# Kernel optimization log

Measured on AMD Instinct MI355X. Metric: run time of the kernel, lower is better.

Reference implementation:

```python
import jax, jax.numpy as jnp
import numpy as np

N = 50000   # n_nodes
E = 800000  # n_edges (directed)
D = 64      # feature dim (in = hidden = out = 64 per source)


def setup_inputs() -> dict:
    key = jax.random.key(0)
    ks = jax.random.split(key, 16)
    s = 0.1  # init scale
    inp = {
        "x": jax.random.normal(ks[0], (N, D), jnp.float32),
        "edge_index": jax.random.randint(ks[1], (2, E), 0, N),
        # GCNConv 1
        "W1": jax.random.normal(ks[2], (D, 64), jnp.float32) * s,
        "b1": jnp.zeros((64,), jnp.float32),
        # TransformerConv (heads=1): query/key/value + root (skip) linear
        "Wq": jax.random.normal(ks[3], (64, 64), jnp.float32) * s,
        "bq": jnp.zeros((64,), jnp.float32),
        "Wk": jax.random.normal(ks[4], (64, 64), jnp.float32) * s,
        "bk": jnp.zeros((64,), jnp.float32),
        "Wv": jax.random.normal(ks[5], (64, 64), jnp.float32) * s,
        "bv": jnp.zeros((64,), jnp.float32),
        "Ws": jax.random.normal(ks[6], (64, 64), jnp.float32) * s,
        "bs": jnp.zeros((64,), jnp.float32),
        # GCNConv 2
        "W2": jax.random.normal(ks[7], (64, D), jnp.float32) * s,
        "b2": jnp.zeros((D,), jnp.float32),
    }
    return inp


def gcn_conv(x, W, b, src, dst, n):
    """PyG GCNConv: symmetric normalization with self-loops, then scatter-add."""
    xw = x @ W  # [N, F]
    loop = jnp.arange(n)
    src2 = jnp.concatenate([src, loop])
    dst2 = jnp.concatenate([dst, loop])
    deg = jax.ops.segment_sum(jnp.ones(src2.shape[0], xw.dtype), dst2, num_segments=n)
    dinv = jnp.where(deg > 0, jax.lax.rsqrt(deg), 0.0)
    norm = dinv[src2] * dinv[dst2]  # [E+N]
    out = jax.ops.segment_sum(xw[src2] * norm[:, None], dst2, num_segments=n)
    return out + b


def segment_softmax(logits, seg, n):
    m = jax.ops.segment_max(logits, seg, num_segments=n)
    e = jnp.exp(logits - m[seg])
    z = jax.ops.segment_sum(e, seg, num_segments=n)
    return e / z[seg]


def transformer_conv(x, Wq, bq, Wk, bk, Wv, bv, Ws, bs, src, dst, n):
    """PyG TransformerConv (heads=1, concat=True, root_weight=True)."""
    q = x @ Wq + bq  # [N, 64]
    k = x @ Wk + bk
    v = x @ Wv + bv
    scale = jax.lax.rsqrt(jnp.asarray(q.shape[-1], q.dtype))
    logits = jnp.sum(q[dst] * k[src], axis=-1) * scale  # [E]
    alpha = segment_softmax(logits, dst, n)
    aggr = jax.ops.segment_sum(v[src] * alpha[:, None], dst, num_segments=n)
    return aggr + x @ Ws + bs  # root/skip connection


def reference(x, edge_index, W1, b1, Wq, bq, Wk, bk, Wv, bv, Ws, bs, W2, b2):
    src, dst = edge_index[0], edge_index[1]
    n = x.shape[0]
    x1 = jax.nn.relu(gcn_conv(x, W1, b1, src, dst, n))
    x2 = transformer_conv(x1, Wq, bq, Wk, bk, Wv, bv, Ws, bs, src, dst, n)
    x3 = gcn_conv(x2, W2, b2, src, dst, n)
    return x3
```

## Files before the change

kernel.cpp:

```cpp
#include <hip/hip_runtime.h>
#include <math.h>


#define D 64
#define BKT_SHIFT 9
#define CAP 12288
#define CHUNK 4096

__device__ __forceinline__ unsigned short f2bf(float f) {
    unsigned int u = __float_as_uint(f);
    u += 0x7FFFu + ((u >> 16) & 1u);
    return (unsigned short)(u >> 16);
}
#define BF_LO(u) __uint_as_float((u) << 16)
#define BF_HI(u) __uint_as_float((u) & 0xFFFF0000u)


__global__ void init_gcursor(int* __restrict__ gcursor) {
    if (threadIdx.x < 128) gcursor[threadIdx.x] = 0;
}

__global__ __launch_bounds__(256) void binA_kernel(const int* __restrict__ src,
                                                   const int* __restrict__ dst,
                                                   int* __restrict__ gcursor,
                                                   unsigned int* __restrict__ staging,
                                                   int e, int nbkt) {
    __shared__ int cntB[128];
    __shared__ int offB[128];
    __shared__ int curB[128];
    __shared__ int gbase[128];
    __shared__ unsigned int pairs[CHUNK];
    __shared__ unsigned char bkt[CHUNK];

    int t = threadIdx.x;
    int e0 = blockIdx.x * CHUNK;
    int ecnt = min(CHUNK, e - e0);

    if (t < 128) cntB[t] = 0;
    __syncthreads();

    int myS[CHUNK / 256], myD[CHUNK / 256];
    #pragma unroll
    for (int i = 0; i < CHUNK / 256; ++i) {
        int idx = t + 256 * i;
        if (idx < ecnt) {
            myS[i] = src[e0 + idx];
            myD[i] = dst[e0 + idx];
            atomicAdd(&cntB[myD[i] >> BKT_SHIFT], 1);
        }
    }
    __syncthreads();
    if (t < 128) offB[t] = cntB[t];
    __syncthreads();
    for (int off = 1; off < 128; off <<= 1) {
        int add = (t < 128 && t >= off) ? offB[t - off] : 0;
        __syncthreads();
        if (t < 128) offB[t] += add;
        __syncthreads();
    }
    if (t < 128) {
        int excl = offB[t] - cntB[t];
        offB[t] = excl;
        curB[t] = excl;
        if (t < nbkt && cntB[t] > 0) gbase[t] = atomicAdd(&gcursor[t], cntB[t]);
    }
    __syncthreads();
    #pragma unroll
    for (int i = 0; i < CHUNK / 256; ++i) {
        int idx = t + 256 * i;
        if (idx < ecnt) {
            int b = myD[i] >> BKT_SHIFT;
            int p = atomicAdd(&curB[b], 1);
            pairs[p] = ((unsigned int)myD[i] << 16) | (unsigned int)myS[i];
            bkt[p] = (unsigned char)b;
        }
    }
    __syncthreads();
    for (int p = t; p < ecnt; p += 256) {
        int b = bkt[p];
        staging[(size_t)b * CAP + gbase[b] + (p - offB[b])] = pairs[p];
    }
}

__global__ __launch_bounds__(256) void binB_kernel(const int* __restrict__ gcursor,
                                                   const unsigned int* __restrict__ staging,
                                                   unsigned short* __restrict__ esrc,
                                                   int* __restrict__ cnt,
                                                   int* __restrict__ rowptr,
                                                   float* __restrict__ dinv,
                                                   int n, int nbkt) {
    __shared__ int bpre[128];
    __shared__ int c512[512];
    __shared__ int o512[512];
    int t = threadIdx.x;
    int b = blockIdx.x;

    if (t < 128) bpre[t] = (t < nbkt) ? gcursor[t] : 0;
    __syncthreads();
    for (int off = 1; off < 128; off <<= 1) {
        int add = (t < 128 && t >= off) ? bpre[t - off] : 0;
        __syncthreads();
        if (t < 128) bpre[t] += add;
        __syncthreads();
    }
    int base_b = (b == 0) ? 0 : bpre[b - 1];
    int cnt_b = gcursor[b];
    int lo = b << BKT_SHIFT;

    c512[t] = 0; c512[t + 256] = 0;
    __syncthreads();
    const unsigned int* st = staging + (size_t)b * CAP;
    for (int i = t; i < cnt_b; i += 256)
        atomicAdd(&c512[(int)(st[i] >> 16) - lo], 1);
    __syncthreads();
    o512[t] = c512[t]; o512[t + 256] = c512[t + 256];
    __syncthreads();
    for (int off = 1; off < 512; off <<= 1) {
        int a1 = (t >= off) ? o512[t - off] : 0;
        int a2 = o512[t + 256 - off];
        __syncthreads();
        o512[t] += a1; o512[t + 256] += a2;
        __syncthreads();
    }
    int e1 = o512[t] - c512[t];
    int e2 = o512[t + 256] - c512[t + 256];
    __syncthreads();
    o512[t] = e1; o512[t + 256] = e2;
    __syncthreads();
    for (int i = t; i < 512; i += 256) {
        int g = lo + i;
        if (g < n) {
            int c = c512[i];
            cnt[g] = c;
            rowptr[g] = base_b + o512[i];
            dinv[g] = rsqrtf((float)c + 1.0f);
        }
    }
    __syncthreads();
    for (int i = t; i < cnt_b; i += 256) {
        unsigned int pk = st[i];
        int local = (int)(pk >> 16) - lo;
        int p = atomicAdd(&o512[local], 1);
        esrc[base_b + p] = (unsigned short)(pk & 0xFFFFu);
    }
}

__global__ __launch_bounds__(256) void gemm64_bf16s(const float* __restrict__ X,
                                                    const float* __restrict__ W,
                                                    const float* __restrict__ dinv,
                                                    unsigned short* __restrict__ xs, int n) {
    __shared__ float sX[64][68];
    __shared__ float sW[64 * 64];
    int t = threadIdx.x;
    int base = blockIdx.x * 64;
    #pragma unroll
    for (int i = 0; i < 4; ++i) {
        int f = t * 4 + i * 1024;
        *(float4*)&sW[f] = *(const float4*)&W[f];
        int r = f >> 6, c = f & 63;
        int row = base + r;
        float4 xv = (row < n) ? *(const float4*)&X[(size_t)row * D + c]
                              : make_float4(0.f, 0.f, 0.f, 0.f);
        *(float4*)&sX[r][c] = xv;
    }
    __syncthreads();

    int cg = t & 15, rg = t >> 4;
    int j0 = cg * 4, r0 = rg * 4;
    float acc[4][4];
    #pragma unroll
    for (int a = 0; a < 4; ++a)
        #pragma unroll
        for (int c = 0; c < 4; ++c) acc[a][c] = 0.0f;

    #pragma unroll 4
    for (int kk = 0; kk < 64; kk += 4) {
        float4 w0 = *(const float4*)&sW[(kk + 0) * 64 + j0];
        float4 w1 = *(const float4*)&sW[(kk + 1) * 64 + j0];
        float4 w2 = *(const float4*)&sW[(kk + 2) * 64 + j0];
        float4 w3 = *(const float4*)&sW[(kk + 3) * 64 + j0];
        #pragma unroll
        for (int a = 0; a < 4; ++a) {
            float4 xv = *(const float4*)&sX[r0 + a][kk];
            acc[a][0] = fmaf(xv.x, w0.x, acc[a][0]); acc[a][1] = fmaf(xv.x, w0.y, acc[a][1]);
            acc[a][2] = fmaf(xv.x, w0.z, acc[a][2]); acc[a][3] = fmaf(xv.x, w0.w, acc[a][3]);
            acc[a][0] = fmaf(xv.y, w1.x, acc[a][0]); acc[a][1] = fmaf(xv.y, w1.y, acc[a][1]);
            acc[a][2] = fmaf(xv.y, w1.z, acc[a][2]); acc[a][3] = fmaf(xv.y, w1.w, acc[a][3]);
            acc[a][0] = fmaf(xv.z, w2.x, acc[a][0]); acc[a][1] = fmaf(xv.z, w2.y, acc[a][1]);
            acc[a][2] = fmaf(xv.z, w2.z, acc[a][2]); acc[a][3] = fmaf(xv.z, w2.w, acc[a][3]);
            acc[a][0] = fmaf(xv.w, w3.x, acc[a][0]); acc[a][1] = fmaf(xv.w, w3.y, acc[a][1]);
            acc[a][2] = fmaf(xv.w, w3.z, acc[a][2]); acc[a][3] = fmaf(xv.w, w3.w, acc[a][3]);
        }
    }

    #pragma unroll
    for (int a = 0; a < 4; ++a) {
        int row = base + r0 + a;
        if (row < n) {
            float dv = dinv[row];
            ushort4 h;
            h.x = f2bf(acc[a][0] * dv);
            h.y = f2bf(acc[a][1] * dv);
            h.z = f2bf(acc[a][2] * dv);
            h.w = f2bf(acc[a][3] * dv);
            *(ushort4*)&xs[(size_t)row * D + j0] = h;
        }
    }
}

__global__ __launch_bounds__(256) void gemm_qkvs(const float* __restrict__ X,
                                                 const float* __restrict__ Wq,
                                                 const float* __restrict__ bq,
                                                 const float* __restrict__ Wk,
                                                 const float* __restrict__ bk,
                                                 const float* __restrict__ Wv,
                                                 const float* __restrict__ bv,
                                                 const float* __restrict__ Ws,
                                                 const float* __restrict__ bs,
                                                 float* __restrict__ Yq,
                                                 unsigned short* __restrict__ kv,
                                                 float* __restrict__ Ysk, int n) {
    __shared__ float sX[64][68];
    __shared__ float sW[64 * 64];
    int t = threadIdx.x;
    int base = blockIdx.x * 64;
    #pragma unroll
    for (int i = 0; i < 4; ++i) {
        int f = t * 4 + i * 1024;
        int r = f >> 6, c = f & 63;
        int row = base + r;
        float4 xv = (row < n) ? *(const float4*)&X[(size_t)row * D + c]
                              : make_float4(0.f, 0.f, 0.f, 0.f);
        *(float4*)&sX[r][c] = xv;
    }

    int cg = t & 15, rg = t >> 4;
    int j0 = cg * 4, r0 = rg * 4;

    #pragma unroll 1
    for (int w4 = 0; w4 < 4; ++w4) {
        const float* W = (w4 == 0) ? Wq : (w4 == 1) ? Wk : (w4 == 2) ? Wv : Ws;
        const float* B = (w4 == 0) ? bq : (w4 == 1) ? bk : (w4 == 2) ? bv : bs;
        __syncthreads();
        #pragma unroll
        for (int i = 0; i < 4; ++i) {
            int f = t * 4 + i * 1024;
            *(float4*)&sW[f] = *(const float4*)&W[f];
        }
        __syncthreads();

        float acc[4][4];
        #pragma unroll
        for (int a = 0; a < 4; ++a)
            #pragma unroll
            for (int c = 0; c < 4; ++c) acc[a][c] = 0.0f;

        #pragma unroll 4
        for (int kk = 0; kk < 64; kk += 4) {
            float4 w0 = *(const float4*)&sW[(kk + 0) * 64 + j0];
            float4 w1 = *(const float4*)&sW[(kk + 1) * 64 + j0];
            float4 w2 = *(const float4*)&sW[(kk + 2) * 64 + j0];
            float4 w3 = *(const float4*)&sW[(kk + 3) * 64 + j0];
            #pragma unroll
            for (int a = 0; a < 4; ++a) {
                float4 xv = *(const float4*)&sX[r0 + a][kk];
                acc[a][0] = fmaf(xv.x, w0.x, acc[a][0]); acc[a][1] = fmaf(xv.x, w0.y, acc[a][1]);
                acc[a][2] = fmaf(xv.x, w0.z, acc[a][2]); acc[a][3] = fmaf(xv.x, w0.w, acc[a][3]);
                acc[a][0] = fmaf(xv.y, w1.x, acc[a][0]); acc[a][1] = fmaf(xv.y, w1.y, acc[a][1]);
                acc[a][2] = fmaf(xv.y, w1.z, acc[a][2]); acc[a][3] = fmaf(xv.y, w1.w, acc[a][3]);
                acc[a][0] = fmaf(xv.z, w2.x, acc[a][0]); acc[a][1] = fmaf(xv.z, w2.y, acc[a][1]);
                acc[a][2] = fmaf(xv.z, w2.z, acc[a][2]); acc[a][3] = fmaf(xv.z, w2.w, acc[a][3]);
                acc[a][0] = fmaf(xv.w, w3.x, acc[a][0]); acc[a][1] = fmaf(xv.w, w3.y, acc[a][1]);
                acc[a][2] = fmaf(xv.w, w3.z, acc[a][2]); acc[a][3] = fmaf(xv.w, w3.w, acc[a][3]);
            }
        }

        float4 bb = *(const float4*)&B[j0];
        if (w4 == 0) {
            #pragma unroll
            for (int a = 0; a < 4; ++a) {
                int row = base + r0 + a;
                if (row < n) {
                    float4 o = make_float4((acc[a][0] + bb.x) * 0.125f,
                                           (acc[a][1] + bb.y) * 0.125f,
                                           (acc[a][2] + bb.z) * 0.125f,
                                           (acc[a][3] + bb.w) * 0.125f);
                    *(float4*)&Yq[(size_t)row * D + j0] = o;
                }
            }
        } else if (w4 == 3) {
            #pragma unroll
            for (int a = 0; a < 4; ++a) {
                int row = base + r0 + a;
                if (row < n) {
                    float4 o = make_float4(acc[a][0] + bb.x, acc[a][1] + bb.y,
                                           acc[a][2] + bb.z, acc[a][3] + bb.w);
                    *(float4*)&Ysk[(size_t)row * D + j0] = o;
                }
            }
        } else {
            int off = (w4 == 1) ? 0 : 64;
            #pragma unroll
            for (int a = 0; a < 4; ++a) {
                int row = base + r0 + a;
                if (row < n) {
                    ushort4 h;
                    h.x = f2bf(acc[a][0] + bb.x);
                    h.y = f2bf(acc[a][1] + bb.y);
                    h.z = f2bf(acc[a][2] + bb.z);
                    h.w = f2bf(acc[a][3] + bb.w);
                    *(ushort4*)&kv[(size_t)row * 128 + off + j0] = h;
                }
            }
        }
    }
}

__global__ __launch_bounds__(256) void gcn_gather_kernel(const unsigned short* __restrict__ xs,
                                                         const float* __restrict__ dinv,
                                                         const int* __restrict__ rowptr,
                                                         const int* __restrict__ cnt,
                                                         const unsigned short* __restrict__ esrc,
                                                         const float* __restrict__ bias,
                                                         float* __restrict__ out,
                                                         int n, int relu) {
    int node = (blockIdx.x * blockDim.x + threadIdx.x) >> 6;
    if (node >= n) return;
    int lane = threadIdx.x & 63;
    int grp = lane >> 3;
    int sub = lane & 7;
    int j0 = sub * 8;

    int start = rowptr[node], deg = cnt[node];

    float a[8] = {0.f, 0.f, 0.f, 0.f, 0.f, 0.f, 0.f, 0.f};
    int i = grp;
    int sNext = (i < deg) ? esrc[start + i] : 0;
    for (; i < deg; i += 8) {
        int s = sNext;
        int in = i + 8;
        if (in < deg) sNext = esrc[start + in];
        uint4 r = *(const uint4*)&xs[(size_t)s * D + j0];
        a[0] += BF_LO(r.x); a[1] += BF_HI(r.x);
        a[2] += BF_LO(r.y); a[3] += BF_HI(r.y);
        a[4] += BF_LO(r.z); a[5] += BF_HI(r.z);
        a[6] += BF_LO(r.w); a[7] += BF_HI(r.w);
    }
    #pragma unroll
    for (int off = 8; off < 64; off <<= 1) {
        #pragma unroll
        for (int c = 0; c < 8; ++c) a[c] += __shfl_xor(a[c], off, 64);
    }

    if (grp == 0) {
        float dd = dinv[node];
        uint4 sr = *(const uint4*)&xs[(size_t)node * D + j0];
        a[0] += BF_LO(sr.x); a[1] += BF_HI(sr.x);
        a[2] += BF_LO(sr.y); a[3] += BF_HI(sr.y);
        a[4] += BF_LO(sr.z); a[5] += BF_HI(sr.z);
        a[6] += BF_LO(sr.w); a[7] += BF_HI(sr.w);
        float4 b0 = *(const float4*)&bias[j0];
        float4 b1 = *(const float4*)&bias[j0 + 4];
        float o[8];
        o[0] = fmaf(dd, a[0], b0.x); o[1] = fmaf(dd, a[1], b0.y);
        o[2] = fmaf(dd, a[2], b0.z); o[3] = fmaf(dd, a[3], b0.w);
        o[4] = fmaf(dd, a[4], b1.x); o[5] = fmaf(dd, a[5], b1.y);
        o[6] = fmaf(dd, a[6], b1.z); o[7] = fmaf(dd, a[7], b1.w);
        if (relu) {
            #pragma unroll
            for (int c = 0; c < 8; ++c) o[c] = fmaxf(o[c], 0.f);
        }
        *(float4*)&out[(size_t)node * D + j0] = make_float4(o[0], o[1], o[2], o[3]);
        *(float4*)&out[(size_t)node * D + j0 + 4] = make_float4(o[4], o[5], o[6], o[7]);
    }
}

__global__ __launch_bounds__(256) void attn_gather_kernel(const float* __restrict__ q,
                                                          const unsigned short* __restrict__ kv,
                                                          const float* __restrict__ skip,
                                                          const int* __restrict__ rowptr,
                                                          const int* __restrict__ cnt,
                                                          const unsigned short* __restrict__ esrc,
                                                          float* __restrict__ out, int n) {
    int node = (blockIdx.x * blockDim.x + threadIdx.x) >> 6;
    if (node >= n) return;
    int lane = threadIdx.x & 63;
    int grp = lane >> 3;
    int sub = lane & 7;
    int j0 = sub * 8;

    int start = rowptr[node], deg = cnt[node];
    float4 q0 = *(const float4*)&q[(size_t)node * D + j0];
    float4 q1 = *(const float4*)&q[(size_t)node * D + j0 + 4];

    float m = -INFINITY, z = 0.0f;
    float a[8] = {0.f, 0.f, 0.f, 0.f, 0.f, 0.f, 0.f, 0.f};

    int i = grp;
    int sNext = (i < deg) ? esrc[start + i] : 0;
    for (; i < deg; i += 8) {
        int s = sNext;
        int in = i + 8;
        if (in < deg) sNext = esrc[start + in];
        const unsigned short* row = kv + (size_t)s * 128;
        uint4 kr = *(const uint4*)&row[j0];
        uint4 vr = *(const uint4*)&row[64 + j0];
        float p = q0.x * BF_LO(kr.x) + q0.y * BF_HI(kr.x)
                + q0.z * BF_LO(kr.y) + q0.w * BF_HI(kr.y)
                + q1.x * BF_LO(kr.z) + q1.y * BF_HI(kr.z)
                + q1.z * BF_LO(kr.w) + q1.w * BF_HI(kr.w);
        p += __shfl_xor(p, 1, 64);
        p += __shfl_xor(p, 2, 64);
        p += __shfl_xor(p, 4, 64);
        float l = p;
        float mn = fmaxf(m, l);
        float corr = __expf(m - mn);
        float w = __expf(l - mn);
        z = z * corr + w;
        a[0] = fmaf(w, BF_LO(vr.x), a[0] * corr);
        a[1] = fmaf(w, BF_HI(vr.x), a[1] * corr);
        a[2] = fmaf(w, BF_LO(vr.y), a[2] * corr);
        a[3] = fmaf(w, BF_HI(vr.y), a[3] * corr);
        a[4] = fmaf(w, BF_LO(vr.z), a[4] * corr);
        a[5] = fmaf(w, BF_HI(vr.z), a[5] * corr);
        a[6] = fmaf(w, BF_LO(vr.w), a[6] * corr);
        a[7] = fmaf(w, BF_HI(vr.w), a[7] * corr);
        m = mn;
    }

    float4 s0 = (grp == 0) ? *(const float4*)&skip[(size_t)node * D + j0]
                           : make_float4(0.f, 0.f, 0.f, 0.f);
    float4 s1 = (grp == 0) ? *(const float4*)&skip[(size_t)node * D + j0 + 4]
                           : make_float4(0.f, 0.f, 0.f, 0.f);

    if (deg > 0) {
        float M = m;
        M = fmaxf(M, __shfl_xor(M, 8, 64));
        M = fmaxf(M, __shfl_xor(M, 16, 64));
        M = fmaxf(M, __shfl_xor(M, 32, 64));
        float sc = __expf(m - M);
        float zs = z * sc;
        #pragma unroll
        for (int c = 0; c < 8; ++c) a[c] *= sc;
        #pragma unroll
        for (int off = 8; off < 64; off <<= 1) {
            zs += __shfl_xor(zs, off, 64);
            #pragma unroll
            for (int c = 0; c < 8; ++c) a[c] += __shfl_xor(a[c], off, 64);
        }
        if (grp == 0) {
            float inv = 1.0f / zs;
            float4 o0, o1;
            o0.x = fmaf(a[0], inv, s0.x); o0.y = fmaf(a[1], inv, s0.y);
            o0.z = fmaf(a[2], inv, s0.z); o0.w = fmaf(a[3], inv, s0.w);
            o1.x = fmaf(a[4], inv, s1.x); o1.y = fmaf(a[5], inv, s1.y);
            o1.z = fmaf(a[6], inv, s1.z); o1.w = fmaf(a[7], inv, s1.w);
            *(float4*)&out[(size_t)node * D + j0] = o0;
            *(float4*)&out[(size_t)node * D + j0 + 4] = o1;
        }
    } else if (grp == 0) {
        *(float4*)&out[(size_t)node * D + j0] = s0;
        *(float4*)&out[(size_t)node * D + j0 + 4] = s1;
    }
}


extern "C" void kernel_launch(void* const* d_in, const int* in_sizes, int n_in,
                              void* d_out, int out_size, void* d_ws, size_t ws_size,
                              hipStream_t stream) {
    const float* x  = (const float*)d_in[0];
    const int*   ei = (const int*)d_in[1];
    const float* W1 = (const float*)d_in[2];
    const float* b1 = (const float*)d_in[3];
    const float* Wq = (const float*)d_in[4];
    const float* bq = (const float*)d_in[5];
    const float* Wk = (const float*)d_in[6];
    const float* bk = (const float*)d_in[7];
    const float* Wv = (const float*)d_in[8];
    const float* bv = (const float*)d_in[9];
    const float* Ws = (const float*)d_in[10];
    const float* bs = (const float*)d_in[11];
    const float* W2 = (const float*)d_in[12];
    const float* b2 = (const float*)d_in[13];
    float* out = (float*)d_out;

    const int n = in_sizes[0] / D;
    const int e = in_sizes[1] / 2;
    const int* src = ei;
    const int* dst = ei + e;
    const int n64 = n * D;
    const int nbkt = (n + (1 << BKT_SHIFT) - 1) >> BKT_SHIFT;

    char* w = (char*)d_ws;
    auto carve = [&](size_t bytes) {
        char* p = w;
        w += (bytes + 255) & ~(size_t)255;
        return p;
    };
    int* gcursor            = (int*)carve(128 * 4);
    unsigned int* staging   = (unsigned int*)carve((size_t)nbkt * CAP * 4);
    unsigned short* esrc    = (unsigned short*)carve((size_t)e * 2);
    int* cnt                = (int*)carve((size_t)n * 4);
    int* rowptr             = (int*)carve((size_t)n * 4);
    float* dinv             = (float*)carve((size_t)n * 4);
    float* bufA             = (float*)carve((size_t)n64 * 4);
    float* bufB             = (float*)carve((size_t)n64 * 4);
    unsigned short* xs      = (unsigned short*)carve((size_t)n64 * 2);
    unsigned short* kv      = (unsigned short*)carve((size_t)n64 * 4);

    const int nb_binA = (e + CHUNK - 1) / CHUNK;
    const int nb_nw   = (n + 3) / 4;
    const int nb_g    = (n + 63) / 64;

    init_gcursor<<<1, 128, 0, stream>>>(gcursor);
    binA_kernel<<<nb_binA, 256, 0, stream>>>(src, dst, gcursor, staging, e, nbkt);
    binB_kernel<<<nbkt, 256, 0, stream>>>(gcursor, staging, esrc, cnt, rowptr, dinv, n, nbkt);

    gemm64_bf16s<<<nb_g, 256, 0, stream>>>(x, W1, dinv, xs, n);
    gcn_gather_kernel<<<nb_nw, 256, 0, stream>>>(xs, dinv, rowptr, cnt, esrc,
                                                 b1, bufB, n, 1);

    gemm_qkvs<<<nb_g, 256, 0, stream>>>(bufB, Wq, bq, Wk, bk, Wv, bv, Ws, bs,
                                        bufA, kv, out, n);
    attn_gather_kernel<<<nb_nw, 256, 0, stream>>>(bufA, kv, out,
                                                  rowptr, cnt, esrc, bufB, n);

    gemm64_bf16s<<<nb_g, 256, 0, stream>>>(bufB, W2, dinv, xs, n);
    gcn_gather_kernel<<<nb_nw, 256, 0, stream>>>(xs, dinv, rowptr, cnt, esrc,
                                                 b2, out, n, 0);
}
```

Before: 254.9 us.

## Fuse GCN/attention gathers into the following GEMM kernels per 64-node tile

The first GCN aggregation (with bias and ReLU) is fused into the Q/K/V/skip GEMM, and the attention aggregation is fused into the W2 GEMM. Each gathered 64-node tile goes straight into shared memory instead of round-tripping full fp32 node-feature buffers through global memory, and two launches are removed. Each node is now handled by 8 lanes that walk all of its edges serially, where before 64 lanes split a node's edges across 8 groups. That gives longer dependent gather loops and fewer waves to hide memory latency.

```diff
diff --git a/kernel.cpp b/kernel.cpp
--- a/kernel.cpp
+++ b/kernel.cpp
@@ -208,34 +208,74 @@
     }
 }
 
-__global__ __launch_bounds__(256) void gemm_qkvs(const float* __restrict__ X,
-                                                 const float* __restrict__ Wq,
-                                                 const float* __restrict__ bq,
-                                                 const float* __restrict__ Wk,
-                                                 const float* __restrict__ bk,
-                                                 const float* __restrict__ Wv,
-                                                 const float* __restrict__ bv,
-                                                 const float* __restrict__ Ws,
-                                                 const float* __restrict__ bs,
-                                                 float* __restrict__ Yq,
-                                                 unsigned short* __restrict__ kv,
-                                                 float* __restrict__ Ysk, int n) {
+__global__ __launch_bounds__(256) void fusedA_kernel(const unsigned short* __restrict__ xs,
+                                                     const float* __restrict__ dinv,
+                                                     const int* __restrict__ rowptr,
+                                                     const int* __restrict__ cnt,
+                                                     const unsigned short* __restrict__ esrc,
+                                                     const float* __restrict__ b1,
+                                                     const float* __restrict__ Wq,
+                                                     const float* __restrict__ bq,
+                                                     const float* __restrict__ Wk,
+                                                     const float* __restrict__ bk,
+                                                     const float* __restrict__ Wv,
+                                                     const float* __restrict__ bv,
+                                                     const float* __restrict__ Ws,
+                                                     const float* __restrict__ bs,
+                                                     float* __restrict__ Yq,
+                                                     unsigned short* __restrict__ kv,
+                                                     float* __restrict__ Ysk, int n) {
     __shared__ float sX[64][68];
     __shared__ float sW[64 * 64];
     int t = threadIdx.x;
     int base = blockIdx.x * 64;
-    #pragma unroll
-    for (int i = 0; i < 4; ++i) {
-        int f = t * 4 + i * 1024;
-        int r = f >> 6, c = f & 63;
-        int row = base + r;
-        float4 xv = (row < n) ? *(const float4*)&X[(size_t)row * D + c]
-                              : make_float4(0.f, 0.f, 0.f, 0.f);
-        *(float4*)&sX[r][c] = xv;
+    int wid = t >> 6, lane = t & 63;
+    int grp = lane >> 3, sub = lane & 7;
+    int j0 = sub * 8;
+
+    float4 bb0 = *(const float4*)&b1[j0];
+    float4 bb1 = *(const float4*)&b1[j0 + 4];
+
+    #pragma unroll
+    for (int slot = 0; slot < 2; ++slot) {
+        int local = wid * 16 + slot * 8 + grp;
+        int node = base + local;
+        float a[8] = {0.f, 0.f, 0.f, 0.f, 0.f, 0.f, 0.f, 0.f};
+        float4 o0 = make_float4(0.f, 0.f, 0.f, 0.f);
+        float4 o1 = make_float4(0.f, 0.f, 0.f, 0.f);
+        if (node < n) {
+            float dd = dinv[node];
+            int start = rowptr[node], deg = cnt[node];
+            uint4 sr = *(const uint4*)&xs[(size_t)node * D + j0];
+            a[0] += BF_LO(sr.x); a[1] += BF_HI(sr.x);
+            a[2] += BF_LO(sr.y); a[3] += BF_HI(sr.y);
+            a[4] += BF_LO(sr.z); a[5] += BF_HI(sr.z);
+            a[6] += BF_LO(sr.w); a[7] += BF_HI(sr.w);
+            int sNext = (deg > 0) ? esrc[start] : 0;
+            for (int i = 0; i < deg; ++i) {
+                int s = sNext;
+                if (i + 1 < deg) sNext = esrc[start + i + 1];
+                uint4 r = *(const uint4*)&xs[(size_t)s * D + j0];
+                a[0] += BF_LO(r.x); a[1] += BF_HI(r.x);
+                a[2] += BF_LO(r.y); a[3] += BF_HI(r.y);
+                a[4] += BF_LO(r.z); a[5] += BF_HI(r.z);
+                a[6] += BF_LO(r.w); a[7] += BF_HI(r.w);
+            }
+            o0.x = fmaxf(fmaf(dd, a[0], bb0.x), 0.f);
+            o0.y = fmaxf(fmaf(dd, a[1], bb0.y), 0.f);
+            o0.z = fmaxf(fmaf(dd, a[2], bb0.z), 0.f);
+            o0.w = fmaxf(fmaf(dd, a[3], bb0.w), 0.f);
+            o1.x = fmaxf(fmaf(dd, a[4], bb1.x), 0.f);
+            o1.y = fmaxf(fmaf(dd, a[5], bb1.y), 0.f);
+            o1.z = fmaxf(fmaf(dd, a[6], bb1.z), 0.f);
+            o1.w = fmaxf(fmaf(dd, a[7], bb1.w), 0.f);
+        }
+        *(float4*)&sX[local][j0] = o0;
+        *(float4*)&sX[local][j0 + 4] = o1;
     }
 
     int cg = t & 15, rg = t >> 4;
-    int j0 = cg * 4, r0 = rg * 4;
+    int gj0 = cg * 4, r0 = rg * 4;
 
     #pragma unroll 1
     for (int w4 = 0; w4 < 4; ++w4) {
@@ -257,10 +297,10 @@
 
         #pragma unroll 4
         for (int kk = 0; kk < 64; kk += 4) {
-            float4 w0 = *(const float4*)&sW[(kk + 0) * 64 + j0];
-            float4 w1 = *(const float4*)&sW[(kk + 1) * 64 + j0];
-            float4 w2 = *(const float4*)&sW[(kk + 2) * 64 + j0];
-            float4 w3 = *(const float4*)&sW[(kk + 3) * 64 + j0];
+            float4 w0 = *(const float4*)&sW[(kk + 0) * 64 + gj0];
+            float4 w1 = *(const float4*)&sW[(kk + 1) * 64 + gj0];
+            float4 w2 = *(const float4*)&sW[(kk + 2) * 64 + gj0];
+            float4 w3 = *(const float4*)&sW[(kk + 3) * 64 + gj0];
             #pragma unroll
             for (int a = 0; a < 4; ++a) {
                 float4 xv = *(const float4*)&sX[r0 + a][kk];
@@ -275,7 +315,7 @@
             }
         }
 
-        float4 bb = *(const float4*)&B[j0];
+        float4 bb = *(const float4*)&B[gj0];
         if (w4 == 0) {
             #pragma unroll
             for (int a = 0; a < 4; ++a) {
@@ -285,7 +325,7 @@
                                            (acc[a][1] + bb.y) * 0.125f,
                                            (acc[a][2] + bb.z) * 0.125f,
                                            (acc[a][3] + bb.w) * 0.125f);
-                    *(float4*)&Yq[(size_t)row * D + j0] = o;
+                    *(float4*)&Yq[(size_t)row * D + gj0] = o;
                 }
             }
         } else if (w4 == 3) {
@@ -295,7 +335,7 @@
                 if (row < n) {
                     float4 o = make_float4(acc[a][0] + bb.x, acc[a][1] + bb.y,
                                            acc[a][2] + bb.z, acc[a][3] + bb.w);
-                    *(float4*)&Ysk[(size_t)row * D + j0] = o;
+                    *(float4*)&Ysk[(size_t)row * D + gj0] = o;
                 }
             }
         } else {
@@ -309,9 +349,132 @@
                     h.y = f2bf(acc[a][1] + bb.y);
                     h.z = f2bf(acc[a][2] + bb.z);
                     h.w = f2bf(acc[a][3] + bb.w);
-                    *(ushort4*)&kv[(size_t)row * 128 + off + j0] = h;
+                    *(ushort4*)&kv[(size_t)row * 128 + off + gj0] = h;
                 }
             }
+        }
+    }
+}
+
+__global__ __launch_bounds__(256) void fusedB_kernel(const float* __restrict__ q,
+                                                     const unsigned short* __restrict__ kv,
+                                                     const float* __restrict__ skip,
+                                                     const float* __restrict__ dinv,
+                                                     const int* __restrict__ rowptr,
+                                                     const int* __restrict__ cnt,
+                                                     const unsigned short* __restrict__ esrc,
+                                                     const float* __restrict__ W2,
+                                                     unsigned short* __restrict__ xs2, int n) {
+    __shared__ float sX[64][68];
+    __shared__ float sW[64 * 64];
+    int t = threadIdx.x;
+    int base = blockIdx.x * 64;
+    int wid = t >> 6, lane = t & 63;
+    int grp = lane >> 3, sub = lane & 7;
+    int j0 = sub * 8;
+
+    #pragma unroll
+    for (int i = 0; i < 4; ++i) {
+        int f = t * 4 + i * 1024;
+        *(float4*)&sW[f] = *(const float4*)&W2[f];
+    }
+
+    #pragma unroll
+    for (int slot = 0; slot < 2; ++slot) {
+        int local = wid * 16 + slot * 8 + grp;
+        int node = base + local;
+        float4 o0 = make_float4(0.f, 0.f, 0.f, 0.f);
+        float4 o1 = make_float4(0.f, 0.f, 0.f, 0.f);
+        if (node < n) {
+            int start = rowptr[node], deg = cnt[node];
+            float4 q0 = *(const float4*)&q[(size_t)node * D + j0];
+            float4 q1 = *(const float4*)&q[(size_t)node * D + j0 + 4];
+            float4 s0 = *(const float4*)&skip[(size_t)node * D + j0];
+            float4 s1 = *(const float4*)&skip[(size_t)node * D + j0 + 4];
+            float m = -INFINITY, z = 0.0f;
+            float a[8] = {0.f, 0.f, 0.f, 0.f, 0.f, 0.f, 0.f, 0.f};
+            int sNext = (deg > 0) ? esrc[start] : 0;
+            for (int i = 0; i < deg; ++i) {
+                int s = sNext;
+                if (i + 1 < deg) sNext = esrc[start + i + 1];
+                const unsigned short* row = kv + (size_t)s * 128;
+                uint4 kr = *(const uint4*)&row[j0];
+                uint4 vr = *(const uint4*)&row[64 + j0];
+                float p = q0.x * BF_LO(kr.x) + q0.y * BF_HI(kr.x)
+                        + q0.z * BF_LO(kr.y) + q0.w * BF_HI(kr.y)
+                        + q1.x * BF_LO(kr.z) + q1.y * BF_HI(kr.z)
+                        + q1.z * BF_LO(kr.w) + q1.w * BF_HI(kr.w);
+                p += __shfl_xor(p, 1, 64);
+                p += __shfl_xor(p, 2, 64);
+                p += __shfl_xor(p, 4, 64);
+                float mn = fmaxf(m, p);
+                float corr = __expf(m - mn);
+                float w = __expf(p - mn);
+                z = z * corr + w;
+                a[0] = fmaf(w, BF_LO(vr.x), a[0] * corr);
+                a[1] = fmaf(w, BF_HI(vr.x), a[1] * corr);
+                a[2] = fmaf(w, BF_LO(vr.y), a[2] * corr);
+                a[3] = fmaf(w, BF_HI(vr.y), a[3] * corr);
+                a[4] = fmaf(w, BF_LO(vr.z), a[4] * corr);
+                a[5] = fmaf(w, BF_HI(vr.z), a[5] * corr);
+                a[6] = fmaf(w, BF_LO(vr.w), a[6] * corr);
+                a[7] = fmaf(w, BF_HI(vr.w), a[7] * corr);
+                m = mn;
+            }
+            if (deg > 0) {
+                float inv = 1.0f / z;
+                o0.x = fmaf(a[0], inv, s0.x); o0.y = fmaf(a[1], inv, s0.y);
+                o0.z = fmaf(a[2], inv, s0.z); o0.w = fmaf(a[3], inv, s0.w);
+                o1.x = fmaf(a[4], inv, s1.x); o1.y = fmaf(a[5], inv, s1.y);
+                o1.z = fmaf(a[6], inv, s1.z); o1.w = fmaf(a[7], inv, s1.w);
+            } else {
+                o0 = s0; o1 = s1;
+            }
+        }
+        *(float4*)&sX[local][j0] = o0;
+        *(float4*)&sX[local][j0 + 4] = o1;
+    }
+    __syncthreads();
+
+    int cg = t & 15, rg = t >> 4;
+    int gj0 = cg * 4, r0 = rg * 4;
+    float acc[4][4];
+    #pragma unroll
+    for (int a = 0; a < 4; ++a)
+        #pragma unroll
+        for (int c = 0; c < 4; ++c) acc[a][c] = 0.0f;
+
+    #pragma unroll 4
+    for (int kk = 0; kk < 64; kk += 4) {
+        float4 w0 = *(const float4*)&sW[(kk + 0) * 64 + gj0];
+        float4 w1 = *(const float4*)&sW[(kk + 1) * 64 + gj0];
+        float4 w2 = *(const float4*)&sW[(kk + 2) * 64 + gj0];
+        float4 w3 = *(const float4*)&sW[(kk + 3) * 64 + gj0];
+        #pragma unroll
+        for (int a = 0; a < 4; ++a) {
+            float4 xv = *(const float4*)&sX[r0 + a][kk];
+            acc[a][0] = fmaf(xv.x, w0.x, acc[a][0]); acc[a][1] = fmaf(xv.x, w0.y, acc[a][1]);
+            acc[a][2] = fmaf(xv.x, w0.z, acc[a][2]); acc[a][3] = fmaf(xv.x, w0.w, acc[a][3]);
+            acc[a][0] = fmaf(xv.y, w1.x, acc[a][0]); acc[a][1] = fmaf(xv.y, w1.y, acc[a][1]);
+            acc[a][2] = fmaf(xv.y, w1.z, acc[a][2]); acc[a][3] = fmaf(xv.y, w1.w, acc[a][3]);
+            acc[a][0] = fmaf(xv.z, w2.x, acc[a][0]); acc[a][1] = fmaf(xv.z, w2.y, acc[a][1]);
+            acc[a][2] = fmaf(xv.z, w2.z, acc[a][2]); acc[a][3] = fmaf(xv.z, w2.w, acc[a][3]);
+            acc[a][0] = fmaf(xv.w, w3.x, acc[a][0]); acc[a][1] = fmaf(xv.w, w3.y, acc[a][1]);
+            acc[a][2] = fmaf(xv.w, w3.z, acc[a][2]); acc[a][3] = fmaf(xv.w, w3.w, acc[a][3]);
+        }
+    }
+
+    #pragma unroll
+    for (int a = 0; a < 4; ++a) {
+        int row = base + r0 + a;
+        if (row < n) {
+            float dv = dinv[row];
+            ushort4 h;
+            h.x = f2bf(acc[a][0] * dv);
+            h.y = f2bf(acc[a][1] * dv);
+            h.z = f2bf(acc[a][2] * dv);
+            h.w = f2bf(acc[a][3] * dv);
+            *(ushort4*)&xs2[(size_t)row * D + gj0] = h;
         }
     }
 }
@@ -372,95 +535,6 @@
         }
         *(float4*)&out[(size_t)node * D + j0] = make_float4(o[0], o[1], o[2], o[3]);
         *(float4*)&out[(size_t)node * D + j0 + 4] = make_float4(o[4], o[5], o[6], o[7]);
-    }
-}
-
-__global__ __launch_bounds__(256) void attn_gather_kernel(const float* __restrict__ q,
-                                                          const unsigned short* __restrict__ kv,
-                                                          const float* __restrict__ skip,
-                                                          const int* __restrict__ rowptr,
-                                                          const int* __restrict__ cnt,
-                                                          const unsigned short* __restrict__ esrc,
-                                                          float* __restrict__ out, int n) {
-    int node = (blockIdx.x * blockDim.x + threadIdx.x) >> 6;
-    if (node >= n) return;
-    int lane = threadIdx.x & 63;
-    int grp = lane >> 3;
-    int sub = lane & 7;
-    int j0 = sub * 8;
-
-    int start = rowptr[node], deg = cnt[node];
-    float4 q0 = *(const float4*)&q[(size_t)node * D + j0];
-    float4 q1 = *(const float4*)&q[(size_t)node * D + j0 + 4];
-
-    float m = -INFINITY, z = 0.0f;
-    float a[8] = {0.f, 0.f, 0.f, 0.f, 0.f, 0.f, 0.f, 0.f};
-
-    int i = grp;
-    int sNext = (i < deg) ? esrc[start + i] : 0;
-    for (; i < deg; i += 8) {
-        int s = sNext;
-        int in = i + 8;
-        if (in < deg) sNext = esrc[start + in];
-        const unsigned short* row = kv + (size_t)s * 128;
-        uint4 kr = *(const uint4*)&row[j0];
-        uint4 vr = *(const uint4*)&row[64 + j0];
-        float p = q0.x * BF_LO(kr.x) + q0.y * BF_HI(kr.x)
-                + q0.z * BF_LO(kr.y) + q0.w * BF_HI(kr.y)
-                + q1.x * BF_LO(kr.z) + q1.y * BF_HI(kr.z)
-                + q1.z * BF_LO(kr.w) + q1.w * BF_HI(kr.w);
-        p += __shfl_xor(p, 1, 64);
-        p += __shfl_xor(p, 2, 64);
-        p += __shfl_xor(p, 4, 64);
-        float l = p;
-        float mn = fmaxf(m, l);
-        float corr = __expf(m - mn);
-        float w = __expf(l - mn);
-        z = z * corr + w;
-        a[0] = fmaf(w, BF_LO(vr.x), a[0] * corr);
-        a[1] = fmaf(w, BF_HI(vr.x), a[1] * corr);
-        a[2] = fmaf(w, BF_LO(vr.y), a[2] * corr);
-        a[3] = fmaf(w, BF_HI(vr.y), a[3] * corr);
-        a[4] = fmaf(w, BF_LO(vr.z), a[4] * corr);
-        a[5] = fmaf(w, BF_HI(vr.z), a[5] * corr);
-        a[6] = fmaf(w, BF_LO(vr.w), a[6] * corr);
-        a[7] = fmaf(w, BF_HI(vr.w), a[7] * corr);
-        m = mn;
-    }
-
-    float4 s0 = (grp == 0) ? *(const float4*)&skip[(size_t)node * D + j0]
-                           : make_float4(0.f, 0.f, 0.f, 0.f);
-    float4 s1 = (grp == 0) ? *(const float4*)&skip[(size_t)node * D + j0 + 4]
-                           : make_float4(0.f, 0.f, 0.f, 0.f);
-
-    if (deg > 0) {
-        float M = m;
-        M = fmaxf(M, __shfl_xor(M, 8, 64));
-        M = fmaxf(M, __shfl_xor(M, 16, 64));
-        M = fmaxf(M, __shfl_xor(M, 32, 64));
-        float sc = __expf(m - M);
-        float zs = z * sc;
-        #pragma unroll
-        for (int c = 0; c < 8; ++c) a[c] *= sc;
-        #pragma unroll
-        for (int off = 8; off < 64; off <<= 1) {
-            zs += __shfl_xor(zs, off, 64);
-            #pragma unroll
-            for (int c = 0; c < 8; ++c) a[c] += __shfl_xor(a[c], off, 64);
-        }
-        if (grp == 0) {
-            float inv = 1.0f / zs;
-            float4 o0, o1;
-            o0.x = fmaf(a[0], inv, s0.x); o0.y = fmaf(a[1], inv, s0.y);
-            o0.z = fmaf(a[2], inv, s0.z); o0.w = fmaf(a[3], inv, s0.w);
-            o1.x = fmaf(a[4], inv, s1.x); o1.y = fmaf(a[5], inv, s1.y);
-            o1.z = fmaf(a[6], inv, s1.z); o1.w = fmaf(a[7], inv, s1.w);
-            *(float4*)&out[(size_t)node * D + j0] = o0;
-            *(float4*)&out[(size_t)node * D + j0 + 4] = o1;
-        }
-    } else if (grp == 0) {
-        *(float4*)&out[(size_t)node * D + j0] = s0;
-        *(float4*)&out[(size_t)node * D + j0 + 4] = s1;
     }
 }
 
@@ -503,8 +577,7 @@
     int* cnt                = (int*)carve((size_t)n * 4);
     int* rowptr             = (int*)carve((size_t)n * 4);
     float* dinv             = (float*)carve((size_t)n * 4);
-    float* bufA             = (float*)carve((size_t)n64 * 4);
-    float* bufB             = (float*)carve((size_t)n64 * 4);
+    float* bufQ             = (float*)carve((size_t)n64 * 4);
     unsigned short* xs      = (unsigned short*)carve((size_t)n64 * 2);
     unsigned short* kv      = (unsigned short*)carve((size_t)n64 * 4);
 
@@ -517,15 +590,14 @@
     binB_kernel<<<nbkt, 256, 0, stream>>>(gcursor, staging, esrc, cnt, rowptr, dinv, n, nbkt);
 
     gemm64_bf16s<<<nb_g, 256, 0, stream>>>(x, W1, dinv, xs, n);
-    gcn_gather_kernel<<<nb_nw, 256, 0, stream>>>(xs, dinv, rowptr, cnt, esrc,
-                                                 b1, bufB, n, 1);
-
-    gemm_qkvs<<<nb_g, 256, 0, stream>>>(bufB, Wq, bq, Wk, bk, Wv, bv, Ws, bs,
-                                        bufA, kv, out, n);
-    attn_gather_kernel<<<nb_nw, 256, 0, stream>>>(bufA, kv, out,
-                                                  rowptr, cnt, esrc, bufB, n);
-
-    gemm64_bf16s<<<nb_g, 256, 0, stream>>>(bufB, W2, dinv, xs, n);
+
+    fusedA_kernel<<<nb_g, 256, 0, stream>>>(xs, dinv, rowptr, cnt, esrc, b1,
+                                            Wq, bq, Wk, bk, Wv, bv, Ws, bs,
+                                            bufQ, kv, out, n);
+
+    fusedB_kernel<<<nb_g, 256, 0, stream>>>(bufQ, kv, out, dinv,
+                                            rowptr, cnt, esrc, W2, xs, n);
+
     gcn_gather_kernel<<<nb_nw, 256, 0, stream>>>(xs, dinv, rowptr, cnt, esrc,
                                                  b2, out, n, 0);
 }
```

Measured after the change: 245.6 us. -3.6%, faster.
